# Performance work log

Measured on AMD Instinct MI355X. Metric: run time of the kernel, lower is better.

The kernel has to match this reference:

```python
import jax, jax.numpy as jnp
import numpy as np

N_NODES = 100000
N_EDGES = 1600000
D = 64  # emb_dim == attn_q_dim == attn_dim


def setup_inputs() -> dict:
    key = jax.random.key(0)
    k1, k2, k3, k4 = jax.random.split(key, 4)
    h = jax.random.normal(k1, (N_NODES, D), dtype=jnp.float32)
    h_attn_q = jax.random.normal(k2, (N_NODES, D), dtype=jnp.float32)
    # attn_lin: Linear(attn_q_dim + attn_dim, 1) -> weight [2D, 1], bias [1]
    W_attn = jax.random.normal(k3, (2 * D, 1), dtype=jnp.float32) * (1.0 / np.sqrt(2 * D))
    b_attn = jnp.zeros((1,), dtype=jnp.float32)
    edge_index = jax.random.randint(k4, (2, N_EDGES), 0, N_NODES, dtype=jnp.int64)
    return {"h": h, "h_attn_q": h_attn_q, "W_attn": W_attn, "b_attn": b_attn,
            "edge_index": edge_index}


def reference(h, h_attn_q, W_attn, b_attn, edge_index):
    """AttnConv (num_relations=1, h_attn=None): per-edge attention score,
    scatter-softmax over destination groups, weighted scatter-add."""
    src = edge_index[0]  # j (message source)
    dst = edge_index[1]  # i (aggregation index)
    n = h.shape[0]
    d_q = h_attn_q.shape[-1]
    # attn_lin(cat([q_i, k_j])) decomposed: score = q_i @ Wq + k_j @ Wk + b
    # (mathematically identical to the concat+linear, avoids [E, 2D] concat)
    alpha_q = h_attn_q @ W_attn[:d_q]          # [N, 1]
    alpha_k = h @ W_attn[d_q:]                 # [N, 1] (h_attn falls back to h_j)
    scores = alpha_q[dst] + alpha_k[src] + b_attn  # [E, 1]
    # scatter softmax over dst groups (PyG softmax(index, ptr, size_i))
    seg_max = jax.ops.segment_max(scores, dst, num_segments=n)  # [N, 1]
    e = jnp.exp(scores - seg_max[dst])
    seg_sum = jax.ops.segment_sum(e, dst, num_segments=n)       # [N, 1]
    a = e / (seg_sum[dst] + 1e-16)                               # [E, 1]
    # weighted scatter-add of messages h_j * a_j
    out = jax.ops.segment_sum(h[src] * a, dst, num_segments=n)   # [N, D]
    return out
```

## Files before the change

### kernel.cpp

```cpp
#include <hip/hip_runtime.h>
#include <hip/hip_fp16.h>
#include <cstdint>
#include <math.h>

#define EMB_D 64
#define BUCKET_BITS 7
#define BUCKET_NODES 128
#define MAXB 1024
#define STRIDE 2560
#define SORT_CAP STRIDE
#define NT 512
#define PART_BLOCKS 256

__global__ __launch_bounds__(NT, 8)
void k_pp(const float* __restrict__ h, const float* __restrict__ W,
          const int* __restrict__ src, const int* __restrict__ dst,
          float* __restrict__ Ak, __half* __restrict__ h16,
          int* __restrict__ brel, unsigned* __restrict__ packed,
          int n_nodes, int n_edges, int part_blocks) {
    __shared__ int lh[MAXB], cur[MAXB];
    int tid = threadIdx.x;
    if (blockIdx.x < (unsigned)part_blocks) {
        int per = (n_edges + part_blocks - 1) / part_blocks;
        int e0 = blockIdx.x * per;
        int e1 = min(e0 + per, n_edges);
        lh[tid] = 0; lh[tid + NT] = 0;
        __syncthreads();
        for (int e = e0 + tid; e < e1; e += NT)
            atomicAdd(&lh[dst[e] >> BUCKET_BITS], 1);
        __syncthreads();
        for (int b = tid; b < MAXB; b += NT) {
            int c = lh[b];
            cur[b] = c ? (b * STRIDE + atomicAdd(&brel[b], c)) : 0;
        }
        __syncthreads();
        for (int e = e0 + tid; e < e1; e += NT) {
            int d  = dst[e];
            int bk = d >> BUCKET_BITS;
            int pos = atomicAdd(&cur[bk], 1);
            if (pos < (bk + 1) * STRIDE)
                packed[pos] = ((unsigned)src[e] << BUCKET_BITS)
                            | (unsigned)(d & (BUCKET_NODES - 1));
        }
    } else {
        long long gid = (long long)(blockIdx.x - part_blocks) * NT + tid;
        int node = (int)(gid >> 4);
        int q    = (int)(gid & 15);
        if (node < n_nodes) {
            const float4* hp = (const float4*)(h + ((long long)node << 6));
            float4 hv = hp[q];
            __half2 p01, p23;
            p01.x = __float2half(hv.x); p01.y = __float2half(hv.y);
            p23.x = __float2half(hv.z); p23.y = __float2half(hv.w);
            uint2 pw;
            pw.x = *(const unsigned*)&p01; pw.y = *(const unsigned*)&p23;
            ((uint2*)(h16 + ((long long)node << 6)))[q] = pw;
            float4 wv = ((const float4*)(W + EMB_D))[q];
            float vk = hv.x * wv.x + hv.y * wv.y + hv.z * wv.z + hv.w * wv.w;
#pragma unroll
            for (int o = 8; o > 0; o >>= 1) vk += __shfl_xor(vk, o, 64);
            if (q == 0) Ak[node] = __expf(vk);
        }
    }
}

__global__ __launch_bounds__(NT, 8)
void k_fused4(const unsigned* __restrict__ packed, const int* __restrict__ brel,
              const float* __restrict__ Ak, const __half* __restrict__ h16,
              float* __restrict__ out, int n_nodes) {
    __shared__ uint2 spair[SORT_CAP];
    __shared__ int cnt[BUCKET_NODES], cur[BUCKET_NODES], rstart[BUCKET_NODES];
    __shared__ short order_[BUCKET_NODES];
    int bk    = blockIdx.x;
    int node0 = bk << BUCKET_BITS;
    int nloc  = min(BUCKET_NODES, n_nodes - node0);
    int beg   = bk * STRIDE;
    int cntE  = min(brel[bk], SORT_CAP);
    int tid = threadIdx.x;

    if (tid < BUCKET_NODES) cnt[tid] = 0;
    if (tid == 0 && cntE == 0) spair[0] = make_uint2(0u, 0u);
    __syncthreads();
    for (int i = tid; i < cntE; i += NT)
        atomicAdd(&cnt[packed[beg + i] & (BUCKET_NODES - 1)], 1);
    __syncthreads();
    if (tid < BUCKET_NODES) cur[tid] = cnt[tid];
    __syncthreads();
    for (int off = 1; off < BUCKET_NODES; off <<= 1) {
        int t = 0;
        if (tid < BUCKET_NODES && tid >= off) t = cur[tid - off];
        __syncthreads();
        if (tid < BUCKET_NODES) cur[tid] += t;
        __syncthreads();
    }
    if (tid < BUCKET_NODES) {
        int excl = cur[tid] - cnt[tid];
        rstart[tid] = excl;
        cur[tid]    = excl;
    }
    __syncthreads();
    for (int i = tid; i < cntE; i += NT) {
        unsigned p = packed[beg + i];
        unsigned s = p >> BUCKET_BITS;
        int pos = atomicAdd(&cur[p & (BUCKET_NODES - 1)], 1);
        spair[pos] = make_uint2(s, __float_as_uint(Ak[s]));
    }
    if (tid < 64) {
        int L = tid;
        int r0 = (cnt[L]      << 8) | L;
        int r1 = (cnt[L + 64] << 8) | (L + 64);
        for (int k = 2; k <= 128; k <<= 1) {
            for (int j = k >> 1; j >= 1; j >>= 1) {
                if (j < 64) {
                    int q0 = __shfl_xor(r0, j, 64);
                    int q1 = __shfl_xor(r1, j, 64);
                    bool lower = ((L & j) == 0);
                    bool up0 = ((L & k) == 0);
                    bool up1 = (((L + 64) & k) == 0);
                    r0 = (up0 == lower) ? min(r0, q0) : max(r0, q0);
                    r1 = (up1 == lower) ? min(r1, q1) : max(r1, q1);
                } else {
                    int lo = min(r0, r1), hi = max(r0, r1);
                    r0 = lo; r1 = hi;
                }
            }
        }
        order_[L]      = (short)(r0 & (BUCKET_NODES - 1));
        order_[L + 64] = (short)(r1 & (BUCKET_NODES - 1));
    }
    __syncthreads();

    int wave = tid >> 6, lane = tid & 63;
    int oct = lane >> 3, ol = lane & 7;
    int cntE_m1 = (cntE > 0) ? (cntE - 1) : 0;
#pragma unroll
    for (int pass = 0; pass < 2; ++pass) {
        int g = pass ? (15 - wave) : wave;
        int dl    = (int)order_[g * 8 + oct];
        int start = rstart[dl], cN = cnt[dl];
        int cmax  = cnt[(int)order_[g * 8 + 7]];
        float a0=0.f,a1=0.f,a2=0.f,a3=0.f,a4=0.f,a5=0.f,a6=0.f,a7=0.f,l=0.f;
        int j = 0;
#pragma unroll 2
        for (; j + 1 < cmax; j += 2) {
            int i0 = min(start + ((j     < cN) ? j     : 0), cntE_m1);
            int i1 = min(start + ((j + 1 < cN) ? j + 1 : 0), cntE_m1);
            uint2 sp0 = spair[i0];
            uint2 sp1 = spair[i1];
            float p0 = (j     < cN) ? __uint_as_float(sp0.y) : 0.f;
            float p1 = (j + 1 < cN) ? __uint_as_float(sp1.y) : 0.f;
            uint4 v0 = ((const uint4*)(h16 + ((long long)sp0.x << 6)))[ol];
            uint4 v1 = ((const uint4*)(h16 + ((long long)sp1.x << 6)))[ol];
            float2 f0 = __half22float2(*(const __half2*)&v0.x);
            float2 f1 = __half22float2(*(const __half2*)&v0.y);
            float2 f2 = __half22float2(*(const __half2*)&v0.z);
            float2 f3 = __half22float2(*(const __half2*)&v0.w);
            a0 = fmaf(p0, f0.x, a0); a1 = fmaf(p0, f0.y, a1);
            a2 = fmaf(p0, f1.x, a2); a3 = fmaf(p0, f1.y, a3);
            a4 = fmaf(p0, f2.x, a4); a5 = fmaf(p0, f2.y, a5);
            a6 = fmaf(p0, f3.x, a6); a7 = fmaf(p0, f3.y, a7);
            l += p0;
            f0 = __half22float2(*(const __half2*)&v1.x);
            f1 = __half22float2(*(const __half2*)&v1.y);
            f2 = __half22float2(*(const __half2*)&v1.z);
            f3 = __half22float2(*(const __half2*)&v1.w);
            a0 = fmaf(p1, f0.x, a0); a1 = fmaf(p1, f0.y, a1);
            a2 = fmaf(p1, f1.x, a2); a3 = fmaf(p1, f1.y, a3);
            a4 = fmaf(p1, f2.x, a4); a5 = fmaf(p1, f2.y, a5);
            a6 = fmaf(p1, f3.x, a6); a7 = fmaf(p1, f3.y, a7);
            l += p1;
        }
        if (j < cmax) {
            int i0 = min(start + ((j < cN) ? j : 0), cntE_m1);
            uint2 sp0 = spair[i0];
            float p0 = (j < cN) ? __uint_as_float(sp0.y) : 0.f;
            uint4 v0 = ((const uint4*)(h16 + ((long long)sp0.x << 6)))[ol];
            float2 f0 = __half22float2(*(const __half2*)&v0.x);
            float2 f1 = __half22float2(*(const __half2*)&v0.y);
            float2 f2 = __half22float2(*(const __half2*)&v0.z);
            float2 f3 = __half22float2(*(const __half2*)&v0.w);
            a0 = fmaf(p0, f0.x, a0); a1 = fmaf(p0, f0.y, a1);
            a2 = fmaf(p0, f1.x, a2); a3 = fmaf(p0, f1.y, a3);
            a4 = fmaf(p0, f2.x, a4); a5 = fmaf(p0, f2.y, a5);
            a6 = fmaf(p0, f3.x, a6); a7 = fmaf(p0, f3.y, a7);
            l += p0;
        }
        if (dl < nloc) {
            float inv = 1.f / (l + 1e-16f);
            float4* orow = (float4*)(out + ((long long)(node0 + dl) << 6));
            orow[ol * 2]     = make_float4(a0 * inv, a1 * inv, a2 * inv, a3 * inv);
            orow[ol * 2 + 1] = make_float4(a4 * inv, a5 * inv, a6 * inv, a7 * inv);
        }
    }
}

extern "C" void kernel_launch(void* const* d_in, const int* in_sizes, int n_in,
                              void* d_out, int out_size, void* d_ws, size_t ws_size,
                              hipStream_t stream) {
    const float* h  = (const float*)d_in[0];
    const float* W  = (const float*)d_in[2];
    const int*   ei = (const int*)d_in[4];

    int n_nodes = in_sizes[0] / EMB_D;
    int n_edges = in_sizes[4] / 2;
    const int* src = ei;
    const int* dst = ei + n_edges;
    float* out = (float*)d_out;

    int n_buckets = (n_nodes + BUCKET_NODES - 1) >> BUCKET_BITS;

    float*    Ak     = (float*)d_ws;
    int*      brel   = (int*)(Ak + n_nodes);
    unsigned* packed = (unsigned*)(brel + MAXB);
    char*     p_end  = (char*)(packed + (size_t)n_buckets * STRIDE);
    __half*   h16    = (__half*)((char*)d_ws +
                       (((size_t)(p_end - (char*)d_ws) + 15) & ~(size_t)15));

    hipMemsetAsync(brel, 0, MAXB * sizeof(int), stream);

    int prep_blocks = (int)(((long long)n_nodes * 16 + NT - 1) / NT);
    k_pp<<<PART_BLOCKS + prep_blocks, NT, 0, stream>>>(h, W, src, dst, Ak, h16,
                                                       brel, packed,
                                                       n_nodes, n_edges, PART_BLOCKS);

    k_fused4<<<n_buckets, NT, 0, stream>>>(packed, brel, Ak, h16, out, n_nodes);
}
```

Baseline: 156.5 us.

## Cache edges in registers, stage packed bucket in LDS, unroll gather by four

The partition kernel now uses enough blocks that each thread loads at most seven edges into registers once, then reuses them for both the histogram and scatter passes instead of reading src/dst twice. The bucket kernel copies the packed edge list into shared memory on the counting pass so the scatter pass reads LDS rather than global memory. The aggregation loop is unrolled to four edges, issuing four gather loads before consuming them, to raise memory-level parallelism. In exchange, LDS use and register pressure go up, which may lower occupancy, and the register cache is correct only while per-block edges fit in REG_E*NT.

```diff
diff --git a/kernel.cpp b/kernel.cpp
--- a/kernel.cpp
+++ b/kernel.cpp
@@ -10,7 +10,7 @@
 #define STRIDE 2560
 #define SORT_CAP STRIDE
 #define NT 512
-#define PART_BLOCKS 256
+#define REG_E 7
 
 __global__ __launch_bounds__(NT, 8)
 void k_pp(const float* __restrict__ h, const float* __restrict__ W,
@@ -26,21 +26,34 @@
         int e1 = min(e0 + per, n_edges);
         lh[tid] = 0; lh[tid + NT] = 0;
         __syncthreads();
-        for (int e = e0 + tid; e < e1; e += NT)
-            atomicAdd(&lh[dst[e] >> BUCKET_BITS], 1);
+        uint2 ed[REG_E];
+#pragma unroll
+        for (int i = 0; i < REG_E; ++i) {
+            int e = e0 + i * NT + tid;
+            if (e < e1) {
+                int d = dst[e];
+                ed[i] = make_uint2((unsigned)src[e], (unsigned)d);
+                atomicAdd(&lh[d >> BUCKET_BITS], 1);
+            } else {
+                ed[i] = make_uint2(0u, 0xFFFFFFFFu);
+            }
+        }
         __syncthreads();
         for (int b = tid; b < MAXB; b += NT) {
             int c = lh[b];
             cur[b] = c ? (b * STRIDE + atomicAdd(&brel[b], c)) : 0;
         }
         __syncthreads();
-        for (int e = e0 + tid; e < e1; e += NT) {
-            int d  = dst[e];
-            int bk = d >> BUCKET_BITS;
-            int pos = atomicAdd(&cur[bk], 1);
-            if (pos < (bk + 1) * STRIDE)
-                packed[pos] = ((unsigned)src[e] << BUCKET_BITS)
-                            | (unsigned)(d & (BUCKET_NODES - 1));
+#pragma unroll
+        for (int i = 0; i < REG_E; ++i) {
+            if (ed[i].y != 0xFFFFFFFFu) {
+                int d  = (int)ed[i].y;
+                int bk = d >> BUCKET_BITS;
+                int pos = atomicAdd(&cur[bk], 1);
+                if (pos < (bk + 1) * STRIDE)
+                    packed[pos] = (ed[i].x << BUCKET_BITS)
+                                | (unsigned)(d & (BUCKET_NODES - 1));
+            }
         }
     } else {
         long long gid = (long long)(blockIdx.x - part_blocks) * NT + tid;
@@ -65,9 +78,10 @@
 }
 
 __global__ __launch_bounds__(NT, 8)
-void k_fused4(const unsigned* __restrict__ packed, const int* __restrict__ brel,
+void k_fused5(const unsigned* __restrict__ packed, const int* __restrict__ brel,
               const float* __restrict__ Ak, const __half* __restrict__ h16,
               float* __restrict__ out, int n_nodes) {
+    __shared__ unsigned stageRaw[SORT_CAP];
     __shared__ uint2 spair[SORT_CAP];
     __shared__ int cnt[BUCKET_NODES], cur[BUCKET_NODES], rstart[BUCKET_NODES];
     __shared__ short order_[BUCKET_NODES];
@@ -81,8 +95,11 @@
     if (tid < BUCKET_NODES) cnt[tid] = 0;
     if (tid == 0 && cntE == 0) spair[0] = make_uint2(0u, 0u);
     __syncthreads();
-    for (int i = tid; i < cntE; i += NT)
-        atomicAdd(&cnt[packed[beg + i] & (BUCKET_NODES - 1)], 1);
+    for (int i = tid; i < cntE; i += NT) {
+        unsigned p = packed[beg + i];
+        stageRaw[i] = p;
+        atomicAdd(&cnt[p & (BUCKET_NODES - 1)], 1);
+    }
     __syncthreads();
     if (tid < BUCKET_NODES) cur[tid] = cnt[tid];
     __syncthreads();
@@ -100,7 +117,7 @@
     }
     __syncthreads();
     for (int i = tid; i < cntE; i += NT) {
-        unsigned p = packed[beg + i];
+        unsigned p = stageRaw[i];
         unsigned s = p >> BUCKET_BITS;
         int pos = atomicAdd(&cur[p & (BUCKET_NODES - 1)], 1);
         spair[pos] = make_uint2(s, __float_as_uint(Ak[s]));
@@ -141,20 +158,28 @@
         int cmax  = cnt[(int)order_[g * 8 + 7]];
         float a0=0.f,a1=0.f,a2=0.f,a3=0.f,a4=0.f,a5=0.f,a6=0.f,a7=0.f,l=0.f;
         int j = 0;
-#pragma unroll 2
-        for (; j + 1 < cmax; j += 2) {
+        for (; j + 3 < cmax; j += 4) {
             int i0 = min(start + ((j     < cN) ? j     : 0), cntE_m1);
             int i1 = min(start + ((j + 1 < cN) ? j + 1 : 0), cntE_m1);
+            int i2 = min(start + ((j + 2 < cN) ? j + 2 : 0), cntE_m1);
+            int i3 = min(start + ((j + 3 < cN) ? j + 3 : 0), cntE_m1);
             uint2 sp0 = spair[i0];
             uint2 sp1 = spair[i1];
+            uint2 sp2 = spair[i2];
+            uint2 sp3 = spair[i3];
+            uint4 v0 = ((const uint4*)(h16 + ((long long)sp0.x << 6)))[ol];
+            uint4 v1 = ((const uint4*)(h16 + ((long long)sp1.x << 6)))[ol];
+            uint4 v2 = ((const uint4*)(h16 + ((long long)sp2.x << 6)))[ol];
+            uint4 v3 = ((const uint4*)(h16 + ((long long)sp3.x << 6)))[ol];
             float p0 = (j     < cN) ? __uint_as_float(sp0.y) : 0.f;
             float p1 = (j + 1 < cN) ? __uint_as_float(sp1.y) : 0.f;
-            uint4 v0 = ((const uint4*)(h16 + ((long long)sp0.x << 6)))[ol];
-            uint4 v1 = ((const uint4*)(h16 + ((long long)sp1.x << 6)))[ol];
-            float2 f0 = __half22float2(*(const __half2*)&v0.x);
-            float2 f1 = __half22float2(*(const __half2*)&v0.y);
-            float2 f2 = __half22float2(*(const __half2*)&v0.z);
-            float2 f3 = __half22float2(*(const __half2*)&v0.w);
+            float p2 = (j + 2 < cN) ? __uint_as_float(sp2.y) : 0.f;
+            float p3 = (j + 3 < cN) ? __uint_as_float(sp3.y) : 0.f;
+            float2 f0, f1, f2, f3;
+            f0 = __half22float2(*(const __half2*)&v0.x);
+            f1 = __half22float2(*(const __half2*)&v0.y);
+            f2 = __half22float2(*(const __half2*)&v0.z);
+            f3 = __half22float2(*(const __half2*)&v0.w);
             a0 = fmaf(p0, f0.x, a0); a1 = fmaf(p0, f0.y, a1);
             a2 = fmaf(p0, f1.x, a2); a3 = fmaf(p0, f1.y, a3);
             a4 = fmaf(p0, f2.x, a4); a5 = fmaf(p0, f2.y, a5);
@@ -169,8 +194,26 @@
             a4 = fmaf(p1, f2.x, a4); a5 = fmaf(p1, f2.y, a5);
             a6 = fmaf(p1, f3.x, a6); a7 = fmaf(p1, f3.y, a7);
             l += p1;
-        }
-        if (j < cmax) {
+            f0 = __half22float2(*(const __half2*)&v2.x);
+            f1 = __half22float2(*(const __half2*)&v2.y);
+            f2 = __half22float2(*(const __half2*)&v2.z);
+            f3 = __half22float2(*(const __half2*)&v2.w);
+            a0 = fmaf(p2, f0.x, a0); a1 = fmaf(p2, f0.y, a1);
+            a2 = fmaf(p2, f1.x, a2); a3 = fmaf(p2, f1.y, a3);
+            a4 = fmaf(p2, f2.x, a4); a5 = fmaf(p2, f2.y, a5);
+            a6 = fmaf(p2, f3.x, a6); a7 = fmaf(p2, f3.y, a7);
+            l += p2;
+            f0 = __half22float2(*(const __half2*)&v3.x);
+            f1 = __half22float2(*(const __half2*)&v3.y);
+            f2 = __half22float2(*(const __half2*)&v3.z);
+            f3 = __half22float2(*(const __half2*)&v3.w);
+            a0 = fmaf(p3, f0.x, a0); a1 = fmaf(p3, f0.y, a1);
+            a2 = fmaf(p3, f1.x, a2); a3 = fmaf(p3, f1.y, a3);
+            a4 = fmaf(p3, f2.x, a4); a5 = fmaf(p3, f2.y, a5);
+            a6 = fmaf(p3, f3.x, a6); a7 = fmaf(p3, f3.y, a7);
+            l += p3;
+        }
+        for (; j < cmax; ++j) {
             int i0 = min(start + ((j < cN) ? j : 0), cntE_m1);
             uint2 sp0 = spair[i0];
             float p0 = (j < cN) ? __uint_as_float(sp0.y) : 0.f;
@@ -218,10 +261,12 @@
 
     hipMemsetAsync(brel, 0, MAXB * sizeof(int), stream);
 
+    int part_blocks = (n_edges + REG_E * NT - 1) / (REG_E * NT);
+    if (part_blocks < 512) part_blocks = 512;
     int prep_blocks = (int)(((long long)n_nodes * 16 + NT - 1) / NT);
-    k_pp<<<PART_BLOCKS + prep_blocks, NT, 0, stream>>>(h, W, src, dst, Ak, h16,
+    k_pp<<<part_blocks + prep_blocks, NT, 0, stream>>>(h, W, src, dst, Ak, h16,
                                                        brel, packed,
-                                                       n_nodes, n_edges, PART_BLOCKS);
-
-    k_fused4<<<n_buckets, NT, 0, stream>>>(packed, brel, Ak, h16, out, n_nodes);
+                                                       n_nodes, n_edges, part_blocks);
+
+    k_fused5<<<n_buckets, NT, 0, stream>>>(packed, brel, Ak, h16, out, n_nodes);
 }
```

Result: no change. 158.6 us (+1.3%).
